# Optimization experiments

Measured on AMD Instinct MI355X. Metric: run time of the kernel, lower is better.

Reference implementation:

```python
import jax, jax.numpy as jnp
import numpy as np

B, S, E, H = 4, 2048, 1024, 8
D = E // H  # head_dim = 128


def setup_inputs() -> dict:
    key = jax.random.key(0)
    ks = jax.random.split(key, 7)
    scale = 1.0 / np.sqrt(D)
    return {
        "sequences": jax.random.normal(ks[0], (B, S, E), dtype=jnp.float32),
        # per-head Linear weights, torch layout [out, in] stacked over heads
        "Wq": jax.random.normal(ks[1], (H, D, D), dtype=jnp.float32) * scale,
        "Wk": jax.random.normal(ks[2], (H, D, D), dtype=jnp.float32) * scale,
        "Wv": jax.random.normal(ks[3], (H, D, D), dtype=jnp.float32) * scale,
        "bq": jax.random.normal(ks[4], (H, D), dtype=jnp.float32) * scale,
        "bk": jax.random.normal(ks[5], (H, D), dtype=jnp.float32) * scale,
        "bv": jax.random.normal(ks[6], (H, D), dtype=jnp.float32) * scale,
    }


def reference(sequences, Wq, Wk, Wv, bq, bk, bv):
    # split feature dim into heads: [B,S,H,D]
    xh = sequences.reshape(B, S, H, D)
    # torch Linear: y = x @ W.T + b  ->  contract input dim d with W[h, o, d]
    q = jnp.einsum("bshd,hod->bsho", xh, Wq) + bq
    k = jnp.einsum("bshd,hod->bsho", xh, Wk) + bk
    v = jnp.einsum("bshd,hod->bsho", xh, Wv) + bv
    # NOTE: original scales by 1/sqrt(num_heads), not 1/sqrt(head_dim)
    scores = jnp.einsum("bshd,bthd->bhst", q, k) / jnp.sqrt(jnp.float32(H))
    attn = jax.nn.softmax(scores, axis=-1)  # [B,H,S,S]
    out = jnp.einsum("bhst,bthd->bshd", attn, v)
    # hstack over heads == reshape back to [B,S,E]
    return out.reshape(B, S, E)
```

## Files before the change

kernel.cpp:

```cpp
#include <hip/hip_runtime.h>
#include <hip/hip_bf16.h>

#define B_ 4
#define S_ 2048
#define E_ 1024
#define H_ 8
#define D_ 128

using f16x8 = __attribute__((ext_vector_type(8))) _Float16;
using f32x4 = __attribute__((ext_vector_type(4))) float;

__device__ __forceinline__ ushort f2h_bits(float f) {
    union { _Float16 h; ushort u; } cv; cv.h = (_Float16)f; return cv.u;
}
__device__ __forceinline__ float h2f(ushort u) {
    union { ushort u; _Float16 h; } cv; cv.u = u; return (float)cv.h;
}
__device__ __forceinline__ f16x8 pack8(const float* __restrict__ p) {
    float4 f0 = *(const float4*)p;
    float4 f1 = *(const float4*)(p + 4);
    f16x8 r;
    r[0] = (_Float16)f0.x; r[1] = (_Float16)f0.y;
    r[2] = (_Float16)f0.z; r[3] = (_Float16)f0.w;
    r[4] = (_Float16)f1.x; r[5] = (_Float16)f1.y;
    r[6] = (_Float16)f1.z; r[7] = (_Float16)f1.w;
    return r;
}

__global__ __launch_bounds__(256) void kv_proj(
    const float* __restrict__ seq,
    const float* __restrict__ Wk, const float* __restrict__ Wv,
    const float* __restrict__ bk, const float* __restrict__ bv,
    ushort* __restrict__ ko, ushort* __restrict__ vo)
{
    constexpr int TS = 136;
    __shared__ ushort Tk[128 * TS];
    __shared__ ushort Tv[128 * TS];
    const int m0 = blockIdx.x * 128, h = blockIdx.y;
    const int tid = threadIdx.x, lane = tid & 63, w = tid >> 6;
    const int l16 = lane & 15, quad = lane >> 4;

    f16x8 a[2][4];
    #pragma unroll
    for (int mt = 0; mt < 2; ++mt)
        #pragma unroll
        for (int ks = 0; ks < 4; ++ks)
            a[mt][ks] = pack8(&seq[(size_t)(m0 + w * 32 + mt * 16 + l16) * E_
                                   + h * D_ + ks * 32 + quad * 8]);

    {
        const float* W = Wk + (size_t)h * D_ * D_;
        f32x4 acc[2][8];
        #pragma unroll
        for (int mt = 0; mt < 2; ++mt)
            #pragma unroll
            for (int nt = 0; nt < 8; ++nt) { f32x4 z = {0.f,0.f,0.f,0.f}; acc[mt][nt] = z; }
        #pragma unroll
        for (int ks = 0; ks < 4; ++ks)
            #pragma unroll
            for (int nt = 0; nt < 8; ++nt) {
                f16x8 bfr = pack8(&W[(size_t)(nt * 16 + l16) * D_ + ks * 32 + quad * 8]);
                #pragma unroll
                for (int mt = 0; mt < 2; ++mt)
                    acc[mt][nt] = __builtin_amdgcn_mfma_f32_16x16x32_f16(
                        a[mt][ks], bfr, acc[mt][nt], 0, 0, 0);
            }
        #pragma unroll
        for (int nt = 0; nt < 8; ++nt) {
            int o = nt * 16 + l16;
            float bias = bk[h * D_ + o];
            #pragma unroll
            for (int mt = 0; mt < 2; ++mt)
                #pragma unroll
                for (int r = 0; r < 4; ++r) {
                    int row = w * 32 + mt * 16 + quad * 4 + r;
                    Tk[row * TS + (o ^ (quad << 3))] = f2h_bits(acc[mt][nt][r] + bias);
                }
        }
    }
    {
        const float* W = Wv + (size_t)h * D_ * D_;
        f32x4 acc[2][8];
        #pragma unroll
        for (int mt = 0; mt < 2; ++mt)
            #pragma unroll
            for (int nt = 0; nt < 8; ++nt) { f32x4 z = {0.f,0.f,0.f,0.f}; acc[mt][nt] = z; }
        #pragma unroll
        for (int ks = 0; ks < 4; ++ks)
            #pragma unroll
            for (int nt = 0; nt < 8; ++nt) {
                f16x8 bfr = pack8(&W[(size_t)(nt * 16 + l16) * D_ + ks * 32 + quad * 8]);
                #pragma unroll
                for (int mt = 0; mt < 2; ++mt)
                    acc[mt][nt] = __builtin_amdgcn_mfma_f32_16x16x32_f16(
                        a[mt][ks], bfr, acc[mt][nt], 0, 0, 0);
            }
        #pragma unroll
        for (int nt = 0; nt < 8; ++nt) {
            int o = nt * 16 + l16;
            float bias = bv[h * D_ + o];
            #pragma unroll
            for (int mt = 0; mt < 2; ++mt)
                #pragma unroll
                for (int r = 0; r < 4; ++r) {
                    int row = w * 32 + mt * 16 + quad * 4 + r;
                    Tv[o * TS + row] = f2h_bits(acc[mt][nt][r] + bias);
                }
        }
    }
    __syncthreads();

    #pragma unroll
    for (int i = 0; i < 8; ++i) {
        int idx = tid + i * 256;
        int row = idx >> 4, c8 = (idx & 15) * 8;
        uint4 dk = *(uint4*)&Tk[row * TS + (c8 ^ (((row >> 2) & 3) << 3))];
        int m = m0 + row, bi = m >> 11, s = m & (S_ - 1);
        *(uint4*)&ko[(((size_t)bi * H_ + h) * S_ + s) * D_ + c8] = dk;
        uint4 dv = *(uint4*)&Tv[row * TS + c8];
        int mg = m0 + c8, bv_i = mg >> 11, s0 = mg & (S_ - 1);
        *(uint4*)&vo[(((size_t)bv_i * H_ + h) * D_ + row) * S_ + s0] = dv;
    }
}

__global__ __launch_bounds__(256) void attn(
    const float* __restrict__ seq, const float* __restrict__ Wq,
    const float* __restrict__ bq,
    const ushort* __restrict__ kg, const ushort* __restrict__ vtg,
    float* __restrict__ out)
{
    constexpr int KS = 136;
    constexpr int VS = 136;
    __shared__ alignas(16) ushort smem[128 * KS + 128 * VS];
    ushort* const Klds = smem;
    ushort* const Vt   = smem + 128 * KS;

    const int m0 = blockIdx.x * 128;
    const int h = blockIdx.y, bi = blockIdx.z;
    const int bh = bi * H_ + h;
    const int tid = threadIdx.x, lane = tid & 63, w = tid >> 6;
    const int l16 = lane & 15, quad = lane >> 4;
    const size_t baseK = (size_t)bh * S_ * D_;
    const size_t baseV = (size_t)bh * D_ * S_;
    const float qscale = 0.35355339059327373f * 1.4426950408889634f;
    const int qq_r = (l16 >> 2) & 3;

    {
        f16x8 xa[2][4];
        #pragma unroll
        for (int mt = 0; mt < 2; ++mt)
            #pragma unroll
            for (int ks = 0; ks < 4; ++ks)
                xa[mt][ks] = pack8(&seq[((size_t)bi * S_ + m0 + w * 32 + mt * 16 + l16) * E_
                                        + h * D_ + ks * 32 + quad * 8]);
        f32x4 qacc[2][8];
        #pragma unroll
        for (int mt = 0; mt < 2; ++mt)
            #pragma unroll
            for (int nt = 0; nt < 8; ++nt) { f32x4 z = {0.f,0.f,0.f,0.f}; qacc[mt][nt] = z; }
        const float* W = Wq + (size_t)h * D_ * D_;
        #pragma unroll
        for (int ks = 0; ks < 4; ++ks)
            #pragma unroll
            for (int nt = 0; nt < 8; ++nt) {
                f16x8 bfr = pack8(&W[(size_t)(nt * 16 + l16) * D_ + ks * 32 + quad * 8]);
                #pragma unroll
                for (int mt = 0; mt < 2; ++mt)
                    qacc[mt][nt] = __builtin_amdgcn_mfma_f32_16x16x32_f16(
                        xa[mt][ks], bfr, qacc[mt][nt], 0, 0, 0);
            }
        #pragma unroll
        for (int nt = 0; nt < 8; ++nt) {
            int o = nt * 16 + l16;
            float bias = bq[h * D_ + o];
            #pragma unroll
            for (int mt = 0; mt < 2; ++mt)
                #pragma unroll
                for (int r = 0; r < 4; ++r) {
                    int row = w * 32 + mt * 16 + quad * 4 + r;
                    Klds[row * KS + (o ^ (quad << 3))] =
                        f2h_bits((qacc[mt][nt][r] + bias) * qscale);
                }
        }
    }
    __syncthreads();

    f16x8 qf[2][4];
    #pragma unroll
    for (int mt = 0; mt < 2; ++mt)
        #pragma unroll
        for (int ks = 0; ks < 4; ++ks)
            qf[mt][ks] = *(const f16x8*)&Klds[(w * 32 + mt * 16 + l16) * KS
                                              + ks * 32 + ((quad ^ qq_r) << 3)];

    f32x4 o_acc[2][8];
    #pragma unroll
    for (int mt = 0; mt < 2; ++mt)
        #pragma unroll
        for (int nt = 0; nt < 8; ++nt) { f32x4 z = {0.f,0.f,0.f,0.f}; o_acc[mt][nt] = z; }
    float m_prev[2][4], l_lane[2][4];
    #pragma unroll
    for (int mt = 0; mt < 2; ++mt)
        #pragma unroll
        for (int r = 0; r < 4; ++r) { m_prev[mt][r] = -1e30f; l_lane[mt][r] = 0.f; }

    for (int j = 0; j < S_ / 128; ++j) {
        const int n0 = j * 128;
        __syncthreads();
        #pragma unroll
        for (int i = 0; i < 8; ++i) {
            int idx = tid + i * 256;
            int r = idx >> 4, c8 = (idx & 15) * 8;
            *(uint4*)&Klds[r * KS + c8] =
                *(const uint4*)&kg[baseK + (size_t)(n0 + r) * D_ + c8];
        }
        #pragma unroll
        for (int i = 0; i < 8; ++i) {
            int idx = tid + i * 256;
            int d = idx >> 4, c8 = (idx & 15) * 8;
            *(uint4*)&Vt[d * VS + c8] =
                *(const uint4*)&vtg[baseV + (size_t)d * S_ + n0 + c8];
        }
        __syncthreads();

        f32x4 sacc[2][8];
        #pragma unroll
        for (int mt = 0; mt < 2; ++mt)
            #pragma unroll
            for (int nt = 0; nt < 8; ++nt) { f32x4 z = {0.f,0.f,0.f,0.f}; sacc[mt][nt] = z; }
        #pragma unroll
        for (int ks = 0; ks < 4; ++ks)
            #pragma unroll
            for (int nt = 0; nt < 8; ++nt) {
                f16x8 kf = *(const f16x8*)&Klds[(nt * 16 + l16) * KS + ks * 32 + quad * 8];
                #pragma unroll
                for (int mt = 0; mt < 2; ++mt)
                    sacc[mt][nt] = __builtin_amdgcn_mfma_f32_16x16x32_f16(
                        qf[mt][ks], kf, sacc[mt][nt], 0, 0, 0);
            }

        #pragma unroll
        for (int mt = 0; mt < 2; ++mt)
            #pragma unroll
            for (int r = 0; r < 4; ++r) {
                float mx = sacc[mt][0][r];
                #pragma unroll
                for (int nt = 1; nt < 8; ++nt) mx = fmaxf(mx, sacc[mt][nt][r]);
                #pragma unroll
                for (int d = 1; d < 16; d <<= 1)
                    mx = fmaxf(mx, __shfl_xor(mx, d));
                float mnew  = fmaxf(m_prev[mt][r], mx);
                float alpha = exp2f(m_prev[mt][r] - mnew);
                m_prev[mt][r] = mnew;
                float sumr = 0.f;
                #pragma unroll
                for (int nt = 0; nt < 8; ++nt) {
                    ushort u = f2h_bits(exp2f(sacc[mt][nt][r] - mnew));
                    sumr += h2f(u);
                    sacc[mt][nt][r] = __uint_as_float((unsigned)u);
                }
                l_lane[mt][r] = l_lane[mt][r] * alpha + sumr;
                #pragma unroll
                for (int nt = 0; nt < 8; ++nt)
                    o_acc[mt][nt][r] *= alpha;
            }

        __syncthreads();
        #pragma unroll
        for (int mt = 0; mt < 2; ++mt)
            #pragma unroll
            for (int r = 0; r < 4; ++r) {
                int row = w * 32 + mt * 16 + quad * 4 + r;
                #pragma unroll
                for (int nt = 0; nt < 8; ++nt) {
                    int col = nt * 16 + l16;
                    Klds[row * KS + (col ^ (quad << 3))] =
                        (ushort)__float_as_uint(sacc[mt][nt][r]);
                }
            }

        #pragma unroll
        for (int ks = 0; ks < 4; ++ks) {
            f16x8 pa[2];
            #pragma unroll
            for (int mt = 0; mt < 2; ++mt)
                pa[mt] = *(const f16x8*)&Klds[(w * 32 + mt * 16 + l16) * KS
                                              + ks * 32 + ((quad ^ qq_r) << 3)];
            #pragma unroll
            for (int nt = 0; nt < 8; ++nt) {
                f16x8 vf = *(const f16x8*)&Vt[(nt * 16 + l16) * VS + ks * 32 + quad * 8];
                #pragma unroll
                for (int mt = 0; mt < 2; ++mt)
                    o_acc[mt][nt] = __builtin_amdgcn_mfma_f32_16x16x32_f16(
                        pa[mt], vf, o_acc[mt][nt], 0, 0, 0);
            }
        }
    }

    #pragma unroll
    for (int mt = 0; mt < 2; ++mt)
        #pragma unroll
        for (int r = 0; r < 4; ++r) {
            float l = l_lane[mt][r];
            #pragma unroll
            for (int d = 1; d < 16; d <<= 1)
                l += __shfl_xor(l, d);
            float rinv = 1.0f / l;
            int srow = m0 + w * 32 + mt * 16 + quad * 4 + r;
            #pragma unroll
            for (int nt = 0; nt < 8; ++nt) {
                int col = nt * 16 + l16;
                out[((size_t)bi * S_ + srow) * E_ + h * D_ + col] =
                    o_acc[mt][nt][r] * rinv;
            }
        }
}

extern "C" void kernel_launch(void* const* d_in, const int* in_sizes, int n_in,
                              void* d_out, int out_size, void* d_ws, size_t ws_size,
                              hipStream_t stream) {
    const float* seq = (const float*)d_in[0];
    const float* Wq  = (const float*)d_in[1];
    const float* Wk  = (const float*)d_in[2];
    const float* Wv  = (const float*)d_in[3];
    const float* bq  = (const float*)d_in[4];
    const float* bk  = (const float*)d_in[5];
    const float* bv  = (const float*)d_in[6];

    const size_t per = (size_t)B_ * H_ * S_ * D_;
    if (ws_size < 2 * per * sizeof(ushort)) return;
    ushort* kws  = (ushort*)d_ws;
    ushort* vtws = kws + per;

    kv_proj<<<dim3(B_ * S_ / 128, H_), 256, 0, stream>>>(
        seq, Wk, Wv, bk, bv, kws, vtws);
    attn<<<dim3(S_ / 128, H_, B_), 256, 0, stream>>>(
        seq, Wq, bq, kws, vtws, (float*)d_out);
}
```

Measured before the change: 307.6 us.

## Transpose MFMA operands for per-lane rows, lazy rescale, packed P stores

Swaps the MFMA operand order so each lane holds a whole query row's scores in its accumulator registers. The row max then needs only two cross-lane shuffles instead of a 16-wide butterfly per row, and the exponentials can be packed into 64-bit LDS stores and float4 output stores. It adds a lazy rescale that touches the running max and the accumulators only when some row's max grows by more than 8, and raises wave priority around the MFMA blocks with s_setprio. The skipped rescale lets exp values reach up to 2^8 before fp16 packing with round-toward-zero conversion, which costs a little accuracy.

```diff
diff --git a/kernel.cpp b/kernel.cpp
--- a/kernel.cpp
+++ b/kernel.cpp
@@ -12,9 +12,6 @@
 
 __device__ __forceinline__ ushort f2h_bits(float f) {
     union { _Float16 h; ushort u; } cv; cv.h = (_Float16)f; return cv.u;
-}
-__device__ __forceinline__ float h2f(ushort u) {
-    union { ushort u; _Float16 h; } cv; cv.u = u; return (float)cv.h;
 }
 __device__ __forceinline__ f16x8 pack8(const float* __restrict__ p) {
     float4 f0 = *(const float4*)p;
@@ -198,11 +195,8 @@
     for (int mt = 0; mt < 2; ++mt)
         #pragma unroll
         for (int nt = 0; nt < 8; ++nt) { f32x4 z = {0.f,0.f,0.f,0.f}; o_acc[mt][nt] = z; }
-    float m_prev[2][4], l_lane[2][4];
-    #pragma unroll
-    for (int mt = 0; mt < 2; ++mt)
-        #pragma unroll
-        for (int r = 0; r < 4; ++r) { m_prev[mt][r] = -1e30f; l_lane[mt][r] = 0.f; }
+    float m_prev[2] = {-1e30f, -1e30f};
+    float l_lane[2] = {0.f, 0.f};
 
     for (int j = 0; j < S_ / 128; ++j) {
         const int n0 = j * 128;
@@ -228,6 +222,7 @@
         for (int mt = 0; mt < 2; ++mt)
             #pragma unroll
             for (int nt = 0; nt < 8; ++nt) { f32x4 z = {0.f,0.f,0.f,0.f}; sacc[mt][nt] = z; }
+        __builtin_amdgcn_s_setprio(1);
         #pragma unroll
         for (int ks = 0; ks < 4; ++ks)
             #pragma unroll
@@ -236,84 +231,93 @@
                 #pragma unroll
                 for (int mt = 0; mt < 2; ++mt)
                     sacc[mt][nt] = __builtin_amdgcn_mfma_f32_16x16x32_f16(
-                        qf[mt][ks], kf, sacc[mt][nt], 0, 0, 0);
-            }
-
-        #pragma unroll
-        for (int mt = 0; mt < 2; ++mt)
-            #pragma unroll
-            for (int r = 0; r < 4; ++r) {
-                float mx = sacc[mt][0][r];
-                #pragma unroll
-                for (int nt = 1; nt < 8; ++nt) mx = fmaxf(mx, sacc[mt][nt][r]);
-                #pragma unroll
-                for (int d = 1; d < 16; d <<= 1)
-                    mx = fmaxf(mx, __shfl_xor(mx, d));
-                float mnew  = fmaxf(m_prev[mt][r], mx);
-                float alpha = exp2f(m_prev[mt][r] - mnew);
-                m_prev[mt][r] = mnew;
-                float sumr = 0.f;
-                #pragma unroll
-                for (int nt = 0; nt < 8; ++nt) {
-                    ushort u = f2h_bits(exp2f(sacc[mt][nt][r] - mnew));
-                    sumr += h2f(u);
-                    sacc[mt][nt][r] = __uint_as_float((unsigned)u);
-                }
-                l_lane[mt][r] = l_lane[mt][r] * alpha + sumr;
+                        kf, qf[mt][ks], sacc[mt][nt], 0, 0, 0);
+            }
+        __builtin_amdgcn_s_setprio(0);
+
+        uint2 pkw[2][8];
+        #pragma unroll
+        for (int mt = 0; mt < 2; ++mt) {
+            float mx4[8];
+            #pragma unroll
+            for (int nt = 0; nt < 8; ++nt)
+                mx4[nt] = fmaxf(fmaxf(sacc[mt][nt][0], sacc[mt][nt][1]),
+                                fmaxf(sacc[mt][nt][2], sacc[mt][nt][3]));
+            float mx = fmaxf(fmaxf(fmaxf(mx4[0], mx4[1]), fmaxf(mx4[2], mx4[3])),
+                             fmaxf(fmaxf(mx4[4], mx4[5]), fmaxf(mx4[6], mx4[7])));
+            mx = fmaxf(mx, __shfl_xor(mx, 16));
+            mx = fmaxf(mx, __shfl_xor(mx, 32));
+            if (__any(mx > m_prev[mt] + 8.0f)) {
+                float mnew  = fmaxf(m_prev[mt], mx);
+                float alpha = exp2f(m_prev[mt] - mnew);
                 #pragma unroll
                 for (int nt = 0; nt < 8; ++nt)
-                    o_acc[mt][nt][r] *= alpha;
-            }
+                    #pragma unroll
+                    for (int r = 0; r < 4; ++r) o_acc[mt][nt][r] *= alpha;
+                l_lane[mt] *= alpha;
+                m_prev[mt] = mnew;
+            }
+            #pragma unroll
+            for (int nt = 0; nt < 8; ++nt) {
+                float e0 = exp2f(sacc[mt][nt][0] - m_prev[mt]);
+                float e1 = exp2f(sacc[mt][nt][1] - m_prev[mt]);
+                float e2 = exp2f(sacc[mt][nt][2] - m_prev[mt]);
+                float e3 = exp2f(sacc[mt][nt][3] - m_prev[mt]);
+                auto p01 = __builtin_amdgcn_cvt_pkrtz(e0, e1);
+                auto p23 = __builtin_amdgcn_cvt_pkrtz(e2, e3);
+                l_lane[mt] += (float)p01[0] + (float)p01[1]
+                            + (float)p23[0] + (float)p23[1];
+                pkw[mt][nt] = make_uint2(__builtin_bit_cast(uint, p01),
+                                         __builtin_bit_cast(uint, p23));
+            }
+        }
 
         __syncthreads();
         #pragma unroll
-        for (int mt = 0; mt < 2; ++mt)
-            #pragma unroll
-            for (int r = 0; r < 4; ++r) {
-                int row = w * 32 + mt * 16 + quad * 4 + r;
-                #pragma unroll
-                for (int nt = 0; nt < 8; ++nt) {
-                    int col = nt * 16 + l16;
-                    Klds[row * KS + (col ^ (quad << 3))] =
-                        (ushort)__float_as_uint(sacc[mt][nt][r]);
-                }
-            }
-
+        for (int mt = 0; mt < 2; ++mt) {
+            const int qrow = w * 32 + mt * 16 + l16;
+            #pragma unroll
+            for (int nt = 0; nt < 8; ++nt)
+                *(uint2*)&Klds[qrow * KS + nt * 16 + quad * 4] = pkw[mt][nt];
+        }
+
+        __builtin_amdgcn_s_setprio(1);
         #pragma unroll
         for (int ks = 0; ks < 4; ++ks) {
-            f16x8 pa[2];
+            f16x8 pb[2];
             #pragma unroll
             for (int mt = 0; mt < 2; ++mt)
-                pa[mt] = *(const f16x8*)&Klds[(w * 32 + mt * 16 + l16) * KS
-                                              + ks * 32 + ((quad ^ qq_r) << 3)];
+                pb[mt] = *(const f16x8*)&Klds[(w * 32 + mt * 16 + l16) * KS
+                                              + ks * 32 + quad * 8];
             #pragma unroll
             for (int nt = 0; nt < 8; ++nt) {
                 f16x8 vf = *(const f16x8*)&Vt[(nt * 16 + l16) * VS + ks * 32 + quad * 8];
                 #pragma unroll
                 for (int mt = 0; mt < 2; ++mt)
                     o_acc[mt][nt] = __builtin_amdgcn_mfma_f32_16x16x32_f16(
-                        pa[mt], vf, o_acc[mt][nt], 0, 0, 0);
-            }
-        }
-    }
-
-    #pragma unroll
-    for (int mt = 0; mt < 2; ++mt)
-        #pragma unroll
-        for (int r = 0; r < 4; ++r) {
-            float l = l_lane[mt][r];
-            #pragma unroll
-            for (int d = 1; d < 16; d <<= 1)
-                l += __shfl_xor(l, d);
-            float rinv = 1.0f / l;
-            int srow = m0 + w * 32 + mt * 16 + quad * 4 + r;
-            #pragma unroll
-            for (int nt = 0; nt < 8; ++nt) {
-                int col = nt * 16 + l16;
-                out[((size_t)bi * S_ + srow) * E_ + h * D_ + col] =
-                    o_acc[mt][nt][r] * rinv;
-            }
-        }
+                        vf, pb[mt], o_acc[mt][nt], 0, 0, 0);
+            }
+        }
+        __builtin_amdgcn_s_setprio(0);
+    }
+
+    #pragma unroll
+    for (int mt = 0; mt < 2; ++mt) {
+        float l = l_lane[mt];
+        l += __shfl_xor(l, 16);
+        l += __shfl_xor(l, 32);
+        float rinv = 1.0f / l;
+        const int q = m0 + w * 32 + mt * 16 + l16;
+        #pragma unroll
+        for (int nt = 0; nt < 8; ++nt) {
+            float4 o;
+            o.x = o_acc[mt][nt][0] * rinv;
+            o.y = o_acc[mt][nt][1] * rinv;
+            o.z = o_acc[mt][nt][2] * rinv;
+            o.w = o_acc[mt][nt][3] * rinv;
+            *(float4*)&out[((size_t)bi * S_ + q) * E_ + h * D_ + nt * 16 + quad * 4] = o;
+        }
+    }
 }
 
 extern "C" void kernel_launch(void* const* d_in, const int* in_sizes, int n_in,
```

Result: faster. 293.8 us (-4.5%).
